# Kernel optimization log

Hardware: AMD Instinct MI355X
Metric: run time of the kernel (lower is better)

Reference implementation:

```python
import jax, jax.numpy as jnp
import numpy as np

KS, STRIDE, PAD = 3, 1, 1
IN_C, OUT_C = 64, 128
EPS = 1e-12
P_SCALE, Q_SCALE = 10.0, 100.0


def unfold2d(x, ks, stride, pad):
    # x: [n, c, h, w] -> [n, c, oh, ow, ks*ks], patch index l = i*ks + j
    x = jnp.pad(x, ((0, 0), (0, 0), (pad, pad), (pad, pad)))
    n, c, H, W = x.shape
    oh = (H - ks) // stride + 1
    ow = (W - ks) // stride + 1
    patches = [x[:, :, i:i + stride * oh:stride, j:j + stride * ow:stride]
               for i in range(ks) for j in range(ks)]
    return jnp.stack(patches, axis=-1)


def setup_inputs() -> dict:
    key = jax.random.key(0)
    k1, k2 = jax.random.split(key)
    x = jax.random.normal(k1, (32, IN_C, 56, 56), dtype=jnp.float32)
    # xavier_uniform over (out, in, ks, ks): bound = sqrt(6/(fan_in+fan_out))
    fan_in = IN_C * KS * KS
    fan_out = OUT_C * KS * KS
    bound = float(np.sqrt(6.0 / (fan_in + fan_out)))
    w = jax.random.uniform(k2, (OUT_C, IN_C, KS * KS), dtype=jnp.float32,
                           minval=-bound, maxval=bound)
    p = jnp.full((OUT_C,), (2.0 ** 0.5) * P_SCALE, dtype=jnp.float32)
    q = jnp.full((1,), 10.0, dtype=jnp.float32)
    return {"x": x, "w": w, "p": p, "q": q}


def reference(x, w, p, q):
    patches = unfold2d(x, KS, STRIDE, PAD)            # [n, c, h, w, l]
    q2 = jnp.square(q / Q_SCALE)                      # [1]
    # patch norms over (c, l)
    x_ss = jnp.sum(jnp.square(patches), axis=(1, 4), keepdims=True)
    x_norm = jnp.sqrt(x_ss + EPS) + q2                # [n,1,h,w,1]
    # weight norms over (c, l)
    w_ss = jnp.sum(jnp.square(w), axis=(1, 2), keepdims=True)
    w_norm = jnp.sqrt(w_ss + EPS) + q2                # [v,1,1]
    out = jnp.einsum('nchwl,vcl->nvhw', patches / x_norm, w / w_norm)
    sign = jnp.sign(out)
    mag = jnp.abs(out) + EPS
    exp = jnp.square(p / P_SCALE).reshape(1, -1, 1, 1)
    return sign * jnp.power(mag, exp)
```

## Files before the change

kernel.cpp:

```cpp
#include <hip/hip_runtime.h>
#include <math.h>
#include <stdint.h>

#define IN_C 64
#define OUT_C 128
#define H 56
#define W 56
#define NB 32
#define HW (H*W)
#define KK 576
#define EPS 1e-12f
#define PH 58
#define PW 66

typedef _Float16 half8 __attribute__((ext_vector_type(8)));
typedef float f32x4 __attribute__((ext_vector_type(4)));

__global__ __launch_bounds__(256) void k_xpose(const float* __restrict__ x,
                                               _Float16* __restrict__ xcl,
                                               float* __restrict__ s) {
    __shared__ float lds[64][59];
    int n = blockIdx.y, pr = blockIdx.x;
    int tid = threadIdx.x;
    int h = pr - 1;
    bool rowz = (h < 0 || h >= H);
    {
        int w = tid & 63, c4 = tid >> 6;
        if (!rowz && w < 56) {
#pragma unroll
            for (int cg = 0; cg < 16; ++cg) {
                int c = cg * 4 + c4;
                lds[c][w] = x[((size_t)(n * IN_C + c)) * HW + h * W + w];
            }
        }
    }
    __syncthreads();
    int c = tid & 63, pg = tid >> 6;
    _Float16* dst = xcl + ((size_t)n * PH + pr) * PW * IN_C;
#pragma unroll
    for (int pcg = 0; pcg < 17; ++pcg) {
        int pc = pcg * 4 + pg;
        if (pc >= PW) break;
        int w = pc - 1;
        bool valid = (!rowz && (unsigned)w < W);
        float val = valid ? lds[c][w] : 0.f;
        dst[(size_t)pc * IN_C + (c ^ ((pc & 7) << 3))] = (_Float16)val;
        float sq = val * val;
#pragma unroll
        for (int off = 32; off > 0; off >>= 1) sq += __shfl_xor(sq, off);
        if (valid && c == 0) s[(size_t)n * HW + h * W + w] = sq;
    }
}

__global__ __launch_bounds__(256) void k_xnorm(const float* __restrict__ s,
                                               const float* __restrict__ q,
                                               float* __restrict__ inv_xn) {
    int t = blockIdx.x * 256 + threadIdx.x;
    if (t >= NB * HW / 4) return;
    int n = t / (HW / 4);
    int rem = t - n * (HW / 4);
    int p0 = rem * 4;
    int h = p0 / W, w0 = p0 - h * W;
    float q2 = q[0] * 0.01f;
    q2 = q2 * q2;
    const float* sp = s + (size_t)n * HW;
    float a0 = 0.f, a1 = 0.f, a2 = 0.f, a3 = 0.f;
#pragma unroll
    for (int dy = -1; dy <= 1; ++dy) {
        int y = h + dy;
        if ((unsigned)y >= H) continue;
        const float* row = sp + y * W;
        float4 m = *(const float4*)(row + w0);
        float lft = (w0 > 0) ? row[w0 - 1] : 0.f;
        float rgt = (w0 + 4 < W) ? row[w0 + 4] : 0.f;
        a0 += lft + m.x + m.y;
        a1 += m.x + m.y + m.z;
        a2 += m.y + m.z + m.w;
        a3 += m.z + m.w + rgt;
    }
    float4 res;
    res.x = 1.f / (sqrtf(a0 + EPS) + q2);
    res.y = 1.f / (sqrtf(a1 + EPS) + q2);
    res.z = 1.f / (sqrtf(a2 + EPS) + q2);
    res.w = 1.f / (sqrtf(a3 + EPS) + q2);
    *(float4*)(inv_xn + (size_t)n * HW + p0) = res;
}

__global__ __launch_bounds__(64) void k_wprep(const float* __restrict__ w,
                                              const float* __restrict__ p,
                                              const float* __restrict__ q,
                                              _Float16* __restrict__ wt,
                                              float* __restrict__ e) {
    int v = blockIdx.x;
    int lane = threadIdx.x;
    const float* wv = w + v * KK;
    float acc = 0.f;
#pragma unroll
    for (int j = 0; j < 9; ++j) {
        float t = wv[lane * 9 + j];
        acc += t * t;
    }
#pragma unroll
    for (int off = 32; off > 0; off >>= 1) acc += __shfl_xor(acc, off);
    float q2 = q[0] * 0.01f;
    q2 = q2 * q2;
    float inv = 1.f / (sqrtf(acc + EPS) + q2);
    int cs = lane ^ ((v & 7) << 3);
#pragma unroll
    for (int l = 0; l < 9; ++l) {
        wt[((size_t)l * OUT_C + v) * IN_C + cs] = (_Float16)(wv[lane * 9 + l] * inv);
    }
    if (lane == 0) e[v] = p[v] * p[v] * 0.01f;
}

__global__ __launch_bounds__(512, 4) void k_conv_mfma(
    const _Float16* __restrict__ xcl,
    const _Float16* __restrict__ wt,
    const float* __restrict__ inv_xn,
    const float* __restrict__ e,
    float* __restrict__ out)
{
    __shared__ __align__(16) _Float16 xls[6 * PW * IN_C];
    __shared__ __align__(16) _Float16 wls[OUT_C * IN_C];

    int tid = threadIdx.x;
    int wv = tid >> 6;
    int lane = tid & 63;
    int l15 = lane & 15;
    int kg = lane >> 4;
    int n = blockIdx.y;
    int r0 = blockIdx.x * 4;
    int row_rel = wv >> 1;
    int vh = wv & 1;

    {
        const float4* src = (const float4*)(xcl + ((size_t)n * PH + r0) * PW * IN_C);
        float4* dstv = (float4*)xls;
#pragma unroll
        for (int i = 0; i < 7; ++i) {
            int off = i * 512 + tid;
            if (off < 6 * PW * IN_C / 8) dstv[off] = src[off];
        }
    }

    float4 wreg0, wreg1;
    {
        const float4* wsrc = (const float4*)wt;
        wreg0 = wsrc[tid];
        wreg1 = wsrc[512 + tid];
    }

    f32x4 acc[4][4];
#pragma unroll
    for (int mt = 0; mt < 4; ++mt)
#pragma unroll
        for (int vt = 0; vt < 4; ++vt) acc[mt][vt] = (f32x4){0.f, 0.f, 0.f, 0.f};

    for (int l = 0; l < 9; ++l) {
        __syncthreads();
        {
            float4* dstv = (float4*)wls;
            dstv[tid] = wreg0;
            dstv[512 + tid] = wreg1;
        }
        if (l < 8) {
            const float4* wsrc = (const float4*)(wt + (size_t)(l + 1) * OUT_C * IN_C);
            wreg0 = wsrc[tid];
            wreg1 = wsrc[512 + tid];
        }
        __syncthreads();

        int di = l / 3, dj = l % 3;
        int pc0 = l15 + dj;
        int xbase = ((row_rel + di) * PW + pc0) * 128;
        int xkey = (pc0 & 7) << 4;
        int wbase = (vh * 64 + l15) * 128;
        int wkey = (l15 & 7) << 4;

#pragma unroll
        for (int k = 0; k < 2; ++k) {
            int koff = k * 64 + kg * 16;
            half8 a[4];
#pragma unroll
            for (int mt = 0; mt < 4; ++mt)
                a[mt] = *(const half8*)((const char*)xls + xbase + mt * 2048 + (koff ^ xkey));
#pragma unroll
            for (int vt = 0; vt < 4; ++vt) {
                half8 b = *(const half8*)((const char*)wls + wbase + vt * 2048 + (koff ^ wkey));
#pragma unroll
                for (int mt = 0; mt < 4; ++mt)
                    acc[mt][vt] = __builtin_amdgcn_mfma_f32_16x16x32_f16(
                        a[mt], b, acc[mt][vt], 0, 0, 0);
            }
        }
    }

    int r = r0 + row_rel;
    const float* ixrow = inv_xn + (size_t)n * HW + r * W;
#pragma unroll
    for (int mt = 0; mt < 4; ++mt) {
        int col0 = mt * 16 + kg * 4;
        if (col0 >= W) continue;
        float4 ixn = *(const float4*)(ixrow + col0);
        const float* ixp = &ixn.x;
#pragma unroll
        for (int vt = 0; vt < 4; ++vt) {
            int v = vh * 64 + vt * 16 + l15;
            float ev = e[v];
            float4 res;
            float* rp = &res.x;
#pragma unroll
            for (int j = 0; j < 4; ++j) {
                float z = acc[mt][vt][j] * ixp[j];
                float mag = fabsf(z) + EPS;
                float pw = exp2f(ev * log2f(mag));
                rp[j] = copysignf(pw, z);
            }
            *(float4*)(out + ((size_t)n * OUT_C + v) * HW + r * W + col0) = res;
        }
    }
}

extern "C" void kernel_launch(void* const* d_in, const int* in_sizes, int n_in,
                              void* d_out, int out_size, void* d_ws, size_t ws_size,
                              hipStream_t stream) {
    const float* x = (const float*)d_in[0];
    const float* w = (const float*)d_in[1];
    const float* p = (const float*)d_in[2];
    const float* q = (const float*)d_in[3];
    float* out = (float*)d_out;

    char* ws = (char*)d_ws;
    float*    s      = (float*)ws;
    float*    inv_xn = (float*)(ws + 401408);
    float*    e      = (float*)(ws + 802816);
    _Float16* wt     = (_Float16*)(ws + 803328);
    _Float16* xcl    = (_Float16*)(ws + 950784);

    k_xpose<<<dim3(PH, NB), dim3(256), 0, stream>>>(x, xcl, s);
    k_xnorm<<<dim3(NB * HW / 4 / 256), dim3(256), 0, stream>>>(s, q, inv_xn);
    k_wprep<<<dim3(OUT_C), dim3(64), 0, stream>>>(w, p, q, wt, e);
    k_conv_mfma<<<dim3(14, NB), dim3(512), 0, stream>>>(xcl, wt, inv_xn, e, out);
}
```

Baseline: 55.41 us.

## Retile conv to 8 rows per block with all nine weight taps resident in LDS

The convolution kernel now splits output channels across blocks: each block handles 8 output rows and 64 output channels, one wave per row. All nine weight taps for that channel half are loaded into LDS once, which removes the per-tap double-sync staging loop. The tap loop is fully unrolled and the A fragments for both K halves are loaded up front. LDS use grows to about 158 KB through dynamic shared memory and launch bounds drop to 2 blocks per CU. This risks lower occupancy, and the input rows are now fetched twice, once for each channel half.

```diff
diff --git a/kernel.cpp b/kernel.cpp
--- a/kernel.cpp
+++ b/kernel.cpp
@@ -12,6 +12,10 @@
 #define EPS 1e-12f
 #define PH 58
 #define PW 66
+
+#define XLS_HALVES (10 * PW * IN_C)
+#define WLS_HALVES (9 * 64 * IN_C)
+#define LDS_BYTES  ((XLS_HALVES + WLS_HALVES) * 2)
 
 typedef _Float16 half8 __attribute__((ext_vector_type(8)));
 typedef float f32x4 __attribute__((ext_vector_type(4)));
@@ -113,42 +117,45 @@
     if (lane == 0) e[v] = p[v] * p[v] * 0.01f;
 }
 
-__global__ __launch_bounds__(512, 4) void k_conv_mfma(
+__global__ __launch_bounds__(512, 2) void k_conv_mfma(
     const _Float16* __restrict__ xcl,
     const _Float16* __restrict__ wt,
     const float* __restrict__ inv_xn,
     const float* __restrict__ e,
     float* __restrict__ out)
 {
-    __shared__ __align__(16) _Float16 xls[6 * PW * IN_C];
-    __shared__ __align__(16) _Float16 wls[OUT_C * IN_C];
+    extern __shared__ __align__(16) char smem[];
+    _Float16* xls = (_Float16*)smem;
+    _Float16* wls = (_Float16*)(smem + XLS_HALVES * 2);
 
     int tid = threadIdx.x;
     int wv = tid >> 6;
     int lane = tid & 63;
     int l15 = lane & 15;
     int kg = lane >> 4;
-    int n = blockIdx.y;
-    int r0 = blockIdx.x * 4;
-    int row_rel = wv >> 1;
-    int vh = wv & 1;
+    int n = blockIdx.z;
+    int vh = blockIdx.y;
+    int r0 = blockIdx.x * 8;
 
     {
         const float4* src = (const float4*)(xcl + ((size_t)n * PH + r0) * PW * IN_C);
-        float4* dstv = (float4*)xls;
-#pragma unroll
-        for (int i = 0; i < 7; ++i) {
-            int off = i * 512 + tid;
-            if (off < 6 * PW * IN_C / 8) dstv[off] = src[off];
-        }
-    }
-
-    float4 wreg0, wreg1;
+        float4* dst = (float4*)xls;
+#pragma unroll
+        for (int i = 0; i < 10; ++i)
+            dst[i * 512 + tid] = src[i * 512 + tid];
+        if (tid < 160)
+            dst[10 * 512 + tid] = src[10 * 512 + tid];
+    }
     {
-        const float4* wsrc = (const float4*)wt;
-        wreg0 = wsrc[tid];
-        wreg1 = wsrc[512 + tid];
-    }
+        float4* dst = (float4*)wls;
+#pragma unroll
+        for (int i = 0; i < 9; ++i) {
+            const float4* src =
+                (const float4*)(wt + ((size_t)i * OUT_C + vh * 64) * IN_C);
+            dst[i * 512 + tid] = src[tid];
+        }
+    }
+    __syncthreads();
 
     f32x4 acc[4][4];
 #pragma unroll
@@ -156,46 +163,40 @@
 #pragma unroll
         for (int vt = 0; vt < 4; ++vt) acc[mt][vt] = (f32x4){0.f, 0.f, 0.f, 0.f};
 
+    const char* xb = (const char*)xls;
+    const char* wb = (const char*)wls;
+
+#pragma unroll
     for (int l = 0; l < 9; ++l) {
-        __syncthreads();
-        {
-            float4* dstv = (float4*)wls;
-            dstv[tid] = wreg0;
-            dstv[512 + tid] = wreg1;
-        }
-        if (l < 8) {
-            const float4* wsrc = (const float4*)(wt + (size_t)(l + 1) * OUT_C * IN_C);
-            wreg0 = wsrc[tid];
-            wreg1 = wsrc[512 + tid];
-        }
-        __syncthreads();
-
         int di = l / 3, dj = l % 3;
         int pc0 = l15 + dj;
-        int xbase = ((row_rel + di) * PW + pc0) * 128;
+        int xbyte = ((wv + di) * PW + pc0) * 128;
         int xkey = (pc0 & 7) << 4;
-        int wbase = (vh * 64 + l15) * 128;
+        int wbyte = l * 8192 + l15 * 128;
         int wkey = (l15 & 7) << 4;
 
+        half8 a[2][4];
+#pragma unroll
+        for (int k = 0; k < 2; ++k)
+#pragma unroll
+            for (int mt = 0; mt < 4; ++mt)
+                a[k][mt] = *(const half8*)(xb + xbyte + mt * 2048
+                                           + ((k * 64 + kg * 16) ^ xkey));
 #pragma unroll
         for (int k = 0; k < 2; ++k) {
-            int koff = k * 64 + kg * 16;
-            half8 a[4];
-#pragma unroll
-            for (int mt = 0; mt < 4; ++mt)
-                a[mt] = *(const half8*)((const char*)xls + xbase + mt * 2048 + (koff ^ xkey));
+            int koff = (k * 64 + kg * 16) ^ wkey;
 #pragma unroll
             for (int vt = 0; vt < 4; ++vt) {
-                half8 b = *(const half8*)((const char*)wls + wbase + vt * 2048 + (koff ^ wkey));
+                half8 b = *(const half8*)(wb + wbyte + vt * 2048 + koff);
 #pragma unroll
                 for (int mt = 0; mt < 4; ++mt)
                     acc[mt][vt] = __builtin_amdgcn_mfma_f32_16x16x32_f16(
-                        a[mt], b, acc[mt][vt], 0, 0, 0);
+                        a[k][mt], b, acc[mt][vt], 0, 0, 0);
             }
         }
     }
 
-    int r = r0 + row_rel;
+    int r = r0 + wv;
     const float* ixrow = inv_xn + (size_t)n * HW + r * W;
 #pragma unroll
     for (int mt = 0; mt < 4; ++mt) {
@@ -237,8 +238,12 @@
     _Float16* wt     = (_Float16*)(ws + 803328);
     _Float16* xcl    = (_Float16*)(ws + 950784);
 
+    hipFuncSetAttribute((const void*)k_conv_mfma,
+                        hipFuncAttributeMaxDynamicSharedMemorySize, LDS_BYTES);
+
     k_xpose<<<dim3(PH, NB), dim3(256), 0, stream>>>(x, xcl, s);
     k_xnorm<<<dim3(NB * HW / 4 / 256), dim3(256), 0, stream>>>(s, q, inv_xn);
     k_wprep<<<dim3(OUT_C), dim3(64), 0, stream>>>(w, p, q, wt, e);
-    k_conv_mfma<<<dim3(14, NB), dim3(512), 0, stream>>>(xcl, wt, inv_xn, e, out);
-}
+    k_conv_mfma<<<dim3(7, 2, NB), dim3(512), LDS_BYTES, stream>>>(
+        xcl, wt, inv_xn, e, out);
+}
```

After: 58.91 us. 1.06x slower.

## Stream conv tiles with direct global-to-LDS loads and double-buffered weights

Applied to the files above, without the earlier changes.

Replaces the register-staged copies of the input tile and per-tap weight slices with direct global_load_lds transfers. Weights are double-buffered so the next tap's slice loads while the current tap computes, which cuts the two barriers per tap to one. The input tile now keeps only the 58 padded columns that are used, both in the transpose kernel and in LDS. Block indices are also swizzled across batches. The kernel switches to dynamic shared memory, and its correctness depends on the wave-uniform LDS destination layout matching the swizzled read pattern.

```diff
diff --git a/kernel.cpp b/kernel.cpp
--- a/kernel.cpp
+++ b/kernel.cpp
@@ -13,8 +13,15 @@
 #define PH 58
 #define PW 66
 
+#define XT_BYTES 44544
+#define WT_BYTES 16384
+#define CONV_LDS (XT_BYTES + 2 * WT_BYTES)
+
 typedef _Float16 half8 __attribute__((ext_vector_type(8)));
 typedef float f32x4 __attribute__((ext_vector_type(4)));
+typedef unsigned int u32;
+typedef const u32 __attribute__((address_space(1)))* gp_t;
+typedef u32 __attribute__((address_space(3)))* sp_t;
 
 __global__ __launch_bounds__(256) void k_xpose(const float* __restrict__ x,
                                                _Float16* __restrict__ xcl,
@@ -38,9 +45,9 @@
     int c = tid & 63, pg = tid >> 6;
     _Float16* dst = xcl + ((size_t)n * PH + pr) * PW * IN_C;
 #pragma unroll
-    for (int pcg = 0; pcg < 17; ++pcg) {
+    for (int pcg = 0; pcg < 15; ++pcg) {
         int pc = pcg * 4 + pg;
-        if (pc >= PW) break;
+        if (pc >= 58) break;
         int w = pc - 1;
         bool valid = (!rowz && (unsigned)w < W);
         float val = valid ? lds[c][w] : 0.f;
@@ -120,35 +127,46 @@
     const float* __restrict__ e,
     float* __restrict__ out)
 {
-    __shared__ __align__(16) _Float16 xls[6 * PW * IN_C];
-    __shared__ __align__(16) _Float16 wls[OUT_C * IN_C];
+    extern __shared__ __align__(16) char smem[];
+    char* xls = smem;
+    char* wls = smem + XT_BYTES;
 
     int tid = threadIdx.x;
     int wv = tid >> 6;
     int lane = tid & 63;
     int l15 = lane & 15;
     int kg = lane >> 4;
-    int n = blockIdx.y;
-    int r0 = blockIdx.x * 4;
+
+    int flat = blockIdx.y * 14 + blockIdx.x;
+    int sw = (flat & 7) * 56 + (flat >> 3);
+    int n = sw / 14;
+    int rc = sw - n * 14;
+    int r0 = rc * 4;
     int row_rel = wv >> 1;
     int vh = wv & 1;
+    int wave_chunk = wv * 64;
 
     {
-        const float4* src = (const float4*)(xcl + ((size_t)n * PH + r0) * PW * IN_C);
-        float4* dstv = (float4*)xls;
-#pragma unroll
-        for (int i = 0; i < 7; ++i) {
-            int off = i * 512 + tid;
-            if (off < 6 * PW * IN_C / 8) dstv[off] = src[off];
-        }
-    }
-
-    float4 wreg0, wreg1;
-    {
-        const float4* wsrc = (const float4*)wt;
-        wreg0 = wsrc[tid];
-        wreg1 = wsrc[512 + tid];
-    }
+        const char* xsrc = (const char*)(xcl + ((size_t)n * PH + r0) * PW * IN_C);
+#pragma unroll
+        for (int i = 0; i < 6; ++i) {
+            int j = i * 512 + tid;
+            if (j < 2784) {
+                int row = j / 464;
+                int off = j - row * 464;
+                __builtin_amdgcn_global_load_lds(
+                    (gp_t)(xsrc + row * (PW * IN_C * 2) + off * 16),
+                    (sp_t)(xls + (i * 512 + wave_chunk) * 16), 16, 0, 0);
+            }
+        }
+        const char* wsrc = (const char*)wt;
+#pragma unroll
+        for (int i = 0; i < 2; ++i)
+            __builtin_amdgcn_global_load_lds(
+                (gp_t)(wsrc + (i * 512 + tid) * 16),
+                (sp_t)(wls + (i * 512 + wave_chunk) * 16), 16, 0, 0);
+    }
+    __syncthreads();
 
     f32x4 acc[4][4];
 #pragma unroll
@@ -156,43 +174,43 @@
 #pragma unroll
         for (int vt = 0; vt < 4; ++vt) acc[mt][vt] = (f32x4){0.f, 0.f, 0.f, 0.f};
 
+#pragma unroll
     for (int l = 0; l < 9; ++l) {
-        __syncthreads();
-        {
-            float4* dstv = (float4*)wls;
-            dstv[tid] = wreg0;
-            dstv[512 + tid] = wreg1;
-        }
         if (l < 8) {
-            const float4* wsrc = (const float4*)(wt + (size_t)(l + 1) * OUT_C * IN_C);
-            wreg0 = wsrc[tid];
-            wreg1 = wsrc[512 + tid];
-        }
-        __syncthreads();
+            const char* wsrc = (const char*)wt + (size_t)(l + 1) * WT_BYTES;
+            char* wdst = wls + ((l + 1) & 1) * WT_BYTES;
+            __builtin_amdgcn_global_load_lds(
+                (gp_t)(wsrc + tid * 16),
+                (sp_t)(wdst + wave_chunk * 16), 16, 0, 0);
+            __builtin_amdgcn_global_load_lds(
+                (gp_t)(wsrc + (512 + tid) * 16),
+                (sp_t)(wdst + (512 + wave_chunk) * 16), 16, 0, 0);
+        }
 
         int di = l / 3, dj = l % 3;
         int pc0 = l15 + dj;
-        int xbase = ((row_rel + di) * PW + pc0) * 128;
+        const char* xb = xls + ((row_rel + di) * 58 + pc0) * 128;
         int xkey = (pc0 & 7) << 4;
-        int wbase = (vh * 64 + l15) * 128;
+        const char* wb = wls + (l & 1) * WT_BYTES + (vh * 64 + l15) * 128;
         int wkey = (l15 & 7) << 4;
 
 #pragma unroll
         for (int k = 0; k < 2; ++k) {
-            int koff = k * 64 + kg * 16;
+            int ko = k * 64 + kg * 16;
             half8 a[4];
 #pragma unroll
             for (int mt = 0; mt < 4; ++mt)
-                a[mt] = *(const half8*)((const char*)xls + xbase + mt * 2048 + (koff ^ xkey));
+                a[mt] = *(const half8*)(xb + mt * 2048 + (ko ^ xkey));
 #pragma unroll
             for (int vt = 0; vt < 4; ++vt) {
-                half8 b = *(const half8*)((const char*)wls + wbase + vt * 2048 + (koff ^ wkey));
+                half8 b = *(const half8*)(wb + vt * 2048 + (ko ^ wkey));
 #pragma unroll
                 for (int mt = 0; mt < 4; ++mt)
                     acc[mt][vt] = __builtin_amdgcn_mfma_f32_16x16x32_f16(
                         a[mt], b, acc[mt][vt], 0, 0, 0);
             }
         }
+        __syncthreads();
     }
 
     int r = r0 + row_rel;
@@ -237,8 +255,12 @@
     _Float16* wt     = (_Float16*)(ws + 803328);
     _Float16* xcl    = (_Float16*)(ws + 950784);
 
+    hipFuncSetAttribute((const void*)k_conv_mfma,
+                        hipFuncAttributeMaxDynamicSharedMemorySize, CONV_LDS);
+
     k_xpose<<<dim3(PH, NB), dim3(256), 0, stream>>>(x, xcl, s);
     k_xnorm<<<dim3(NB * HW / 4 / 256), dim3(256), 0, stream>>>(s, q, inv_xn);
     k_wprep<<<dim3(OUT_C), dim3(64), 0, stream>>>(w, p, q, wt, e);
-    k_conv_mfma<<<dim3(14, NB), dim3(512), 0, stream>>>(xcl, wt, inv_xn, e, out);
-}
+    k_conv_mfma<<<dim3(14, NB), dim3(512), CONV_LDS, stream>>>(
+        xcl, wt, inv_xn, e, out);
+}
```

Result: faster. 52.43 us (-5.4%).
